# Kernel optimization log

Measured on AMD Instinct MI355X. Metric: run time of the kernel, lower is better.

The kernel has to match this reference:

```python
import jax, jax.numpy as jnp
import numpy as np

B, C, H, W = 16, 256, 56, 56
CR = C // 4
PAD = 1
NUM_ITERS = 5


def _conv(x, w, b):
    # NCHW conv, stride 1, 'same' padding for k=3
    y = jax.lax.conv_general_dilated(x, w, (1, 1), [(PAD, PAD), (PAD, PAD)],
                                     dimension_numbers=('NCHW', 'OIHW', 'NCHW'))
    return y + b[None, :, None, None]


_GAUSS = np.array([[1., 2., 1.], [2., 4., 2.], [1., 2., 1.]], np.float32) / 16.0


def _crf_rnn(unary1, compat, spatial_w):
    # Mean-field CRF-RNN refinement with num_labels=2 and a fixed spatial Gaussian kernel.
    unary = jnp.concatenate([unary1, -unary1], axis=1)  # [B,2,h,w] two-label unary from 1-ch map
    gk = jnp.tile(jnp.asarray(_GAUSS)[None, None], (2, 1, 1, 1))  # depthwise [2,1,3,3]
    q = jax.nn.softmax(unary, axis=1)
    for _ in range(NUM_ITERS):
        blur = jax.lax.conv_general_dilated(q, gk, (1, 1), [(1, 1), (1, 1)],
                                            dimension_numbers=('NCHW', 'OIHW', 'NCHW'),
                                            feature_group_count=2)
        msg = blur * spatial_w[None, :, None, None]          # filter-output weighting
        pairwise = jnp.einsum('lk,bkhw->blhw', compat, msg)  # label compatibility transform
        q = jax.nn.softmax(unary - pairwise, axis=1)
    return q[:, 1:2]  # P(label=1) as refined spatial attention map


def _forward(x, w0_0, b0_0, w0_1, b0_1, w0_2, b0_2, w0_3, b0_3, w0_4, b0_4,
             w1, b1, w2, b2, fc1_w, fc2_w, fc2_b, crf_compat, crf_spatial_w):
    f1 = jax.nn.relu(_conv(x, w0_0, b0_0))             # [B,C,H,W]  (dominant compute)
    f1c = jnp.mean(f1, axis=(2, 3), keepdims=True)      # global avg pool -> [B,C,1,1]
    f2 = jax.nn.relu(_conv(f1c, w0_1, b0_1))            # [B,C,1,1]
    v_c = jax.nn.sigmoid(f1c[:, :, 0, 0] @ fc1_w.T)[:, :, None, None]  # channel attention
    f_c = v_c * f2
    f3 = jax.nn.relu(_conv(f_c, w0_2, b0_2))
    f4 = jax.nn.relu(_conv(f3, w0_3, b0_3))
    f3s = jax.nn.relu(_conv(f3, w1, b1))                # [B,C/4,1,1]
    v0s = jax.nn.relu(_conv(f3s, w2, b2))               # [B,1,1,1] initial spatial attention
    v_s = _crf_rnn(v0s, crf_compat, crf_spatial_w)      # CRF-RNN refined attention
    f_s = v_s * f4
    f_r = jax.nn.relu(_conv(f_s, w0_4, b0_4))
    f_ra = jnp.mean(f_r, axis=(2, 3), keepdims=True)    # [B,C,1,1]
    p_n = jax.nn.sigmoid(f_ra[:, :, 0, 0] @ fc2_w.T + fc2_b)  # [B,1]
    return p_n


def setup_inputs() -> dict:
    key = jax.random.key(0)
    ks = jax.random.split(key, 16)

    def w(k, shape, fan):
        return jax.random.normal(k, shape, jnp.float32) / np.sqrt(fan)

    inp = {'x': jax.random.normal(ks[0], (B, C, H, W), jnp.float32)}
    for i in range(5):
        inp['w0_%d' % i] = w(ks[1 + i], (C, C, 3, 3), C * 9)
        inp['b0_%d' % i] = jnp.zeros((C,), jnp.float32)
    inp['w1'] = w(ks[6], (CR, C, 3, 3), C * 9)
    inp['b1'] = jnp.zeros((CR,), jnp.float32)
    inp['w2'] = w(ks[7], (1, CR, 3, 3), CR * 9)
    inp['b2'] = jnp.zeros((1,), jnp.float32)
    inp['fc1_w'] = w(ks[8], (C, C), C)
    inp['fc2_w'] = w(ks[9], (1, C), C)
    inp['fc2_b'] = jnp.zeros((1,), jnp.float32)
    inp['crf_compat'] = jnp.asarray([[0., 1.], [1., 0.]], jnp.float32) + 0.1 * jax.random.normal(ks[10], (2, 2), jnp.float32)
    inp['crf_spatial_w'] = jnp.ones((2,), jnp.float32)
    return inp


def reference(x, w0_0, b0_0, w0_1, b0_1, w0_2, b0_2, w0_3, b0_3, w0_4, b0_4,
              w1, b1, w2, b2, fc1_w, fc2_w, fc2_b, crf_compat, crf_spatial_w):
    return _forward(x, w0_0, b0_0, w0_1, b0_1, w0_2, b0_2, w0_3, b0_3, w0_4, b0_4,
                    w1, b1, w2, b2, fc1_w, fc2_w, fc2_b, crf_compat, crf_spatial_w)
```

## Files before the change

kernel.cpp:

```cpp
#include <hip/hip_runtime.h>
#include <hip/hip_bf16.h>

typedef __bf16 bf16x8 __attribute__((ext_vector_type(8)));
typedef float f32x4 __attribute__((ext_vector_type(4)));

#define NB 16
#define NC 256
#define NHW 3136
#define NW 56
#define PROW 58
#define PPLANE (58 * 58)

#define NRX2 1568
#define NBP 288
#define NMAT 85
#define NHALO 114

__device__ __forceinline__ unsigned short f2bf(float f) {
    union { float f; unsigned u; } v; v.f = f;
    unsigned r = v.u + 0x7FFFu + ((v.u >> 16) & 1u);
    return (unsigned short)(r >> 16);
}

__device__ __forceinline__ void gload_lds16(const void* g, void* l) {
    __builtin_amdgcn_global_load_lds((const __attribute__((address_space(1))) void*)g,
                                     (__attribute__((address_space(3))) void*)l, 16, 0, 0);
}

__global__ void k_prep(const float* __restrict__ x,
                       const float* __restrict__ w0_0, const float* __restrict__ w0_1,
                       const float* __restrict__ w0_2, const float* __restrict__ w0_3,
                       const float* __restrict__ w0_4, const float* __restrict__ w1,
                       const float* __restrict__ w2, const float* __restrict__ fc1_w,
                       unsigned short* __restrict__ xT, unsigned short* __restrict__ Bp,
                       float* __restrict__ w01T, float* __restrict__ w02T,
                       float* __restrict__ w03T, float* __restrict__ w04T,
                       float* __restrict__ fc1T, float* __restrict__ w1T,
                       float* __restrict__ w2c) {
    __shared__ float sh[64 * 65];
    int bid = blockIdx.x, tid = threadIdx.x;

    if (bid < NRX2) {
        int hwb = bid % 98;
        int b = bid / 98;
        int c_l = tid >> 5, hw_l = tid & 31;
        int qd = tid & 7, hw2 = tid >> 3;
        int hw = hwb * 32 + hw2;
        int y = hw / 56, xp = hw - y * 56;
        for (int cb = 0; cb < 8; ++cb) {
            const float* src = x + ((size_t)b * NC + (size_t)cb * 32) * NHW + hwb * 32;
#pragma unroll
            for (int r = 0; r < 4; ++r) {
                int c = c_l + r * 8;
                sh[c * 33 + hw_l] = src[(size_t)c * NHW + hw_l];
            }
            __syncthreads();
            unsigned short* dst = xT + ((size_t)(b * 8 + cb) * PPLANE +
                                        (size_t)(y + 1) * PROW + (xp + 1)) * 32 + qd * 4;
            ushort4 v;
            v.x = f2bf(sh[(qd * 4 + 0) * 33 + hw2]);
            v.y = f2bf(sh[(qd * 4 + 1) * 33 + hw2]);
            v.z = f2bf(sh[(qd * 4 + 2) * 33 + hw2]);
            v.w = f2bf(sh[(qd * 4 + 3) * 33 + hw2]);
            *(ushort4*)dst = v;
            __syncthreads();
        }
        return;
    }
    if (bid < NRX2 + NBP) {
        int bw = bid - NRX2;
#pragma unroll
        for (int k = 0; k < 8; ++k) {
            int idx = (bw * 8 + k) * 256 + tid;
            int q = idx & 31;
            int n = (idx >> 5) & 255;
            int s = idx >> 13;
            int tap = s >> 3;
            int ic = (s & 7) * 32 + q;
            Bp[idx] = f2bf(w0_0[(size_t)n * 2304 + (size_t)ic * 9 + tap]);
        }
        return;
    }
    if (bid < NRX2 + NBP + NMAT) {
        int tb = bid - NRX2 - NBP;
        if (tb < 84) {
            const float* src; float* dst;
            int sstr, estr, off, OD, o0, i0;
            if (tb < 80) {
                int arr = tb >> 4, t16 = tb & 15;
                o0 = (t16 >> 2) * 64; i0 = (t16 & 3) * 64; OD = 256;
                sstr = 2304; estr = 9; off = 4;
                switch (arr) {
                    case 0: src = w0_1; dst = w01T; break;
                    case 1: src = w0_2; dst = w02T; break;
                    case 2: src = w0_3; dst = w03T; break;
                    case 3: src = w0_4; dst = w04T; break;
                    default: src = fc1_w; dst = fc1T; sstr = 256; estr = 1; off = 0; break;
                }
            } else {
                int t4i = tb - 80; o0 = 0; i0 = t4i * 64; OD = 64;
                sstr = 2304; estr = 9; off = 4;
                src = w1; dst = w1T;
            }
            int i1 = tid & 63, o4 = tid >> 6;
#pragma unroll
            for (int p = 0; p < 16; ++p) {
                int oo = p * 4 + o4;
                sh[oo * 65 + i1] = src[(size_t)(o0 + oo) * sstr + (size_t)(i0 + i1) * estr + off];
            }
            __syncthreads();
            int o1 = tid & 63, i4 = tid >> 6;
#pragma unroll
            for (int p = 0; p < 16; ++p) {
                int ii = p * 4 + i4;
                dst[(size_t)(i0 + ii) * OD + o0 + o1] = sh[o1 * 65 + ii];
            }
        } else {
            if (tid < 64) w2c[tid] = w2[tid * 9 + 4];
        }
        return;
    }
    {
        int t = (bid - NRX2 - NBP - NMAT) * 256 + tid;
        if (t >= 128 * 228) return;
        int plane = t / 228, h = t % 228;
        int row, xc;
        if (h < 58)       { row = 0;       xc = h; }
        else if (h < 116) { row = 57;      xc = h - 58; }
        else if (h < 172) { row = h - 115; xc = 0; }
        else              { row = h - 171; xc = 57; }
        size_t e = ((size_t)plane * PPLANE + (size_t)row * PROW + xc) * 32;
        uint4 z = {0u, 0u, 0u, 0u};
        *(uint4*)(xT + e)      = z;
        *(uint4*)(xT + e + 8)  = z;
        *(uint4*)(xT + e + 16) = z;
        *(uint4*)(xT + e + 24) = z;
    }
}

__global__ __launch_bounds__(256, 2) void k_conv(
    const unsigned short* __restrict__ xT,
    const unsigned short* __restrict__ Bp,
    const float* __restrict__ b0_0,
    float* __restrict__ partial) {
    __shared__ __align__(16) char alds[2][16384];
    int lblk = ((blockIdx.x & 7) * 56) + (blockIdx.x >> 3);
    int b = lblk / 28, pt = lblk % 28;
    int tid = threadIdx.x;
    int lane = tid & 63, wave = tid >> 6;
    int col = lane & 15, grp = lane >> 4;
    int nbase = wave * 64;

    int swz = (lane & 3) ^ ((lane >> 3) & 3);
    int pixoff = ((lane >> 2) << 6) + (swz << 4);
    const char* xbytes = (const char*)xT;
    size_t stage_row = (size_t)(pt * 2 + wave) * (PROW * 64);

    int p_[7][3];
#pragma unroll
    for (int mt = 0; mt < 7; ++mt) {
        int q = mt * 16 + col;
        int r = q >= 56 ? 1 : 0;
        int x = q - 56 * r;
#pragma unroll
        for (int dxi = 0; dxi < 3; ++dxi) {
            int ppx = x + dxi;
            int slot = grp ^ ((ppx >> 1) & 3);
            p_[mt][dxi] = r * 4096 + ppx * 64 + slot * 16;
        }
    }
    int boff[4];
#pragma unroll
    for (int nt = 0; nt < 4; ++nt)
        boff[nt] = ((nbase + nt * 16 + col) * 32 + grp * 8) * 2;

    f32x4 acc[7][4];
#pragma unroll
    for (int mt = 0; mt < 7; ++mt)
#pragma unroll
        for (int nt = 0; nt < 4; ++nt) {
            acc[mt][nt][0] = 0.f; acc[mt][nt][1] = 0.f;
            acc[mt][nt][2] = 0.f; acc[mt][nt][3] = 0.f;
        }

    {
        const char* g0 = xbytes + (size_t)(b * 8) * (PPLANE * 64) + stage_row + pixoff;
        char* l0 = &alds[0][wave * 4096];
#pragma unroll
        for (int j = 0; j < 4; ++j)
            gload_lds16(g0 + j * 1024, l0 + j * 1024);
    }
    bf16x8 bcur[4], bnxt[4];
    {
        const char* bp0 = (const char*)Bp;
#pragma unroll
        for (int nt = 0; nt < 4; ++nt)
            bcur[nt] = *(const bf16x8*)(bp0 + boff[nt]);
    }
    __syncthreads();

    for (int icb = 0; icb < 8; ++icb) {
        int cur = icb & 1;
        if (icb < 7) {
            const char* g = xbytes + (size_t)(b * 8 + icb + 1) * (PPLANE * 64) + stage_row + pixoff;
            char* l = &alds[cur ^ 1][wave * 4096];
#pragma unroll
            for (int j = 0; j < 4; ++j)
                gload_lds16(g + j * 1024, l + j * 1024);
        }
        const char* abuf = alds[cur];
#pragma unroll
        for (int tap = 0; tap < 9; ++tap) {
            int nicb = (tap == 8) ? icb + 1 : icb;
            int ntap = (tap == 8) ? 0 : tap + 1;
            if (nicb < 8) {
                const char* bp = (const char*)Bp + ((size_t)(ntap * 8 + nicb) << 13);
#pragma unroll
                for (int nt = 0; nt < 4; ++nt)
                    bnxt[nt] = *(const bf16x8*)(bp + boff[nt]);
            }
            int dyi = tap / 3, dxi = tap % 3;
            bf16x8 af[7];
#pragma unroll
            for (int mt = 0; mt < 7; ++mt)
                af[mt] = *(const bf16x8*)(abuf + (p_[mt][dxi] + dyi * 4096));
#pragma unroll
            for (int mt = 0; mt < 7; ++mt)
#pragma unroll
                for (int nt = 0; nt < 4; ++nt)
                    acc[mt][nt] = __builtin_amdgcn_mfma_f32_16x16x32_bf16(af[mt], bcur[nt], acc[mt][nt], 0, 0, 0);
#pragma unroll
            for (int nt = 0; nt < 4; ++nt) bcur[nt] = bnxt[nt];
        }
        __syncthreads();
    }

#pragma unroll
    for (int nt = 0; nt < 4; ++nt) {
        int n = nbase + nt * 16 + col;
        float bias = b0_0[n];
        float s = 0.f;
#pragma unroll
        for (int mt = 0; mt < 7; ++mt)
#pragma unroll
            for (int j = 0; j < 4; ++j)
                s += fmaxf(acc[mt][nt][j] + bias, 0.f);
        s += __shfl_down(s, 32);
        s += __shfl_down(s, 16);
        if (grp == 0) partial[(size_t)lblk * NC + n] = s;
    }
}

__global__ __launch_bounds__(1024) void k_tail(
    const float* __restrict__ partial,
    const float* __restrict__ w01T, const float* __restrict__ fc1T,
    const float* __restrict__ w02T, const float* __restrict__ w03T,
    const float* __restrict__ w04T, const float* __restrict__ w1T,
    const float* __restrict__ w2c,
    const float* __restrict__ b0_1, const float* __restrict__ b0_2,
    const float* __restrict__ b0_3, const float* __restrict__ b0_4,
    const float* __restrict__ b1, const float* __restrict__ b2,
    const float* __restrict__ fc2_w, const float* __restrict__ fc2_b,
    const float* __restrict__ compat, const float* __restrict__ spatial_w,
    float* __restrict__ out) {
    __shared__ float fc[256], t2[256], t3[256], t4[256];
    __shared__ float rA[4][256], rB[4][256];
    __shared__ float red64[64];
    __shared__ float vs_sh;
    int b = blockIdx.x, tid = threadIdx.x;
    int o = tid & 255, seg = tid >> 8;
    int i0 = seg * 64;

    {
        float s = 0.f;
        const float* pp = partial + (size_t)b * 28 * 256 + o;
#pragma unroll
        for (int r = seg * 7; r < seg * 7 + 7; ++r) s += pp[r * 256];
        rA[seg][o] = s;
    }
    __syncthreads();
    if (seg == 0) fc[o] = (rA[0][o] + rA[1][o] + rA[2][o] + rA[3][o]) * (1.f / 3136.f);
    __syncthreads();

    {
        float a2 = 0.f, av = 0.f;
        for (int i = i0; i < i0 + 64; ++i) {
            float fi = fc[i];
            a2 = fmaf(w01T[i * 256 + o], fi, a2);
            av = fmaf(fc1T[i * 256 + o], fi, av);
        }
        rA[seg][o] = a2; rB[seg][o] = av;
    }
    __syncthreads();
    if (seg == 0) {
        float A = rA[0][o] + rA[1][o] + rA[2][o] + rA[3][o];
        float V = rB[0][o] + rB[1][o] + rB[2][o] + rB[3][o];
        t2[o] = fmaxf(A + b0_1[o], 0.f) / (1.f + expf(-V));
    }
    __syncthreads();

    {
        float a3 = 0.f;
        for (int i = i0; i < i0 + 64; ++i) a3 = fmaf(w02T[i * 256 + o], t2[i], a3);
        rA[seg][o] = a3;
    }
    __syncthreads();
    if (seg == 0) t3[o] = fmaxf(rA[0][o] + rA[1][o] + rA[2][o] + rA[3][o] + b0_2[o], 0.f);
    __syncthreads();

    {
        float a4 = 0.f;
        for (int i = i0; i < i0 + 64; ++i) a4 = fmaf(w03T[i * 256 + o], t3[i], a4);
        rA[seg][o] = a4;
        int o64 = tid & 63, s16 = tid >> 6;
        float a5 = 0.f;
        for (int i = s16 * 16; i < s16 * 16 + 16; ++i) a5 = fmaf(w1T[i * 64 + o64], t3[i], a5);
        ((float*)rB)[s16 * 64 + o64] = a5;
    }
    __syncthreads();
    if (seg == 0) t4[o] = fmaxf(rA[0][o] + rA[1][o] + rA[2][o] + rA[3][o] + b0_3[o], 0.f);
    if (tid < 64) {
        float a5 = 0.f;
        const float* rb = (const float*)rB;
#pragma unroll
        for (int j = 0; j < 16; ++j) a5 += rb[j * 64 + tid];
        float v = fmaxf(a5 + b1[tid], 0.f);
        red64[tid] = v * w2c[tid];
    }
    __syncthreads();
    if (tid == 0) {
        float u = 0.f;
        for (int i = 0; i < 64; ++i) u += red64[i];
        u = fmaxf(u + b2[0], 0.f);
        float c00 = compat[0], c01 = compat[1], c10 = compat[2], c11 = compat[3];
        float sw0 = spatial_w[0], sw1 = spatial_w[1];
        float q1 = 1.f / (1.f + expf(2.f * u));
        float q0 = 1.f - q1;
        for (int it = 0; it < 5; ++it) {
            float m0 = q0 * 0.25f * sw0;
            float m1 = q1 * 0.25f * sw1;
            float pw0 = c00 * m0 + c01 * m1;
            float pw1 = c10 * m0 + c11 * m1;
            float z0 = u - pw0, z1 = -u - pw1;
            q1 = 1.f / (1.f + expf(z0 - z1));
            q0 = 1.f - q1;
        }
        vs_sh = q1;
    }
    __syncthreads();

    {
        float a6 = 0.f;
        for (int i = i0; i < i0 + 64; ++i) a6 = fmaf(w04T[i * 256 + o], t4[i], a6);
        rA[seg][o] = a6;
    }
    __syncthreads();
    if (seg == 0) {
        float A = rA[0][o] + rA[1][o] + rA[2][o] + rA[3][o];
        float fr = fmaxf(vs_sh * A + b0_4[o], 0.f);
        rB[0][o] = fr * fc2_w[o];
    }
    __syncthreads();
    if (tid < 128) rB[0][tid] += rB[0][tid + 128];
    __syncthreads();
    if (tid < 64) rB[0][tid] += rB[0][tid + 64];
    __syncthreads();
    if (tid == 0) {
        float t = 0.f;
        for (int i = 0; i < 64; ++i) t += rB[0][i];
        out[b] = 1.f / (1.f + expf(-(t + fc2_b[0])));
    }
}

extern "C" void kernel_launch(void* const* d_in, const int* in_sizes, int n_in,
                              void* d_out, int out_size, void* d_ws, size_t ws_size,
                              hipStream_t stream) {
    const float* x     = (const float*)d_in[0];
    const float* w0_0  = (const float*)d_in[1];
    const float* b0_0  = (const float*)d_in[2];
    const float* w0_1  = (const float*)d_in[3];
    const float* b0_1  = (const float*)d_in[4];
    const float* w0_2  = (const float*)d_in[5];
    const float* b0_2  = (const float*)d_in[6];
    const float* w0_3  = (const float*)d_in[7];
    const float* b0_3  = (const float*)d_in[8];
    const float* w0_4  = (const float*)d_in[9];
    const float* b0_4  = (const float*)d_in[10];
    const float* w1    = (const float*)d_in[11];
    const float* b1    = (const float*)d_in[12];
    const float* w2    = (const float*)d_in[13];
    const float* b2    = (const float*)d_in[14];
    const float* fc1_w = (const float*)d_in[15];
    const float* fc2_w = (const float*)d_in[16];
    const float* fc2_b = (const float*)d_in[17];
    const float* compat = (const float*)d_in[18];
    const float* sw     = (const float*)d_in[19];

    unsigned short* xT = (unsigned short*)d_ws;
    unsigned short* Bp = xT + (size_t)128 * PPLANE * 32;
    float* w01T = (float*)(Bp + 589824);
    float* w02T = w01T + 65536;
    float* w03T = w02T + 65536;
    float* w04T = w03T + 65536;
    float* fc1T = w04T + 65536;
    float* w1T  = fc1T + 65536;
    float* w2c  = w1T + 16384;
    float* partial = w2c + 64;

    hipLaunchKernelGGL(k_prep, dim3(NRX2 + NBP + NMAT + NHALO), dim3(256), 0, stream,
                       x, w0_0, w0_1, w0_2, w0_3, w0_4, w1, w2, fc1_w,
                       xT, Bp, w01T, w02T, w03T, w04T, fc1T, w1T, w2c);
    hipLaunchKernelGGL(k_conv, dim3(448), dim3(256), 0, stream, xT, Bp, b0_0, partial);
    hipLaunchKernelGGL(k_tail, dim3(16), dim3(1024), 0, stream, partial,
                       w01T, fc1T, w02T, w03T, w04T, w1T, w2c,
                       b0_1, b0_2, b0_3, b0_4, b1, b2, fc2_w, fc2_b, compat, sw,
                       (float*)d_out);
}
```

Before: 201.8 us.

## Split prep into finer blocks and triple-buffer B fragments with MFMA priority

```diff
diff --git a/kernel.cpp b/kernel.cpp
--- a/kernel.cpp
+++ b/kernel.cpp
@@ -11,9 +11,8 @@
 #define PROW 58
 #define PPLANE (58 * 58)
 
-#define NRX2 1568
-#define NBP 288
-#define NMAT 85
+#define NRX 12544
+#define NRW 2389
 #define NHALO 114
 
 __device__ __forceinline__ unsigned short f2bf(float f) {
@@ -40,21 +39,24 @@
     __shared__ float sh[64 * 65];
     int bid = blockIdx.x, tid = threadIdx.x;
 
-    if (bid < NRX2) {
+    if (bid < NRX) {
         int hwb = bid % 98;
-        int b = bid / 98;
-        int c_l = tid >> 5, hw_l = tid & 31;
-        int qd = tid & 7, hw2 = tid >> 3;
-        int hw = hwb * 32 + hw2;
-        int y = hw / 56, xp = hw - y * 56;
-        for (int cb = 0; cb < 8; ++cb) {
+        int cb = (bid / 98) % 8;
+        int b = bid / (98 * 8);
+        {
+            int c_l = tid >> 5, hw_l = tid & 31;
             const float* src = x + ((size_t)b * NC + (size_t)cb * 32) * NHW + hwb * 32;
 #pragma unroll
             for (int r = 0; r < 4; ++r) {
                 int c = c_l + r * 8;
                 sh[c * 33 + hw_l] = src[(size_t)c * NHW + hw_l];
             }
-            __syncthreads();
+        }
+        __syncthreads();
+        {
+            int qd = tid & 7, hw2 = tid >> 3;
+            int hw = hwb * 32 + hw2;
+            int y = hw / 56, xp = hw - y * 56;
             unsigned short* dst = xT + ((size_t)(b * 8 + cb) * PPLANE +
                                         (size_t)(y + 1) * PROW + (xp + 1)) * 32 + qd * 4;
             ushort4 v;
@@ -63,26 +65,22 @@
             v.z = f2bf(sh[(qd * 4 + 2) * 33 + hw2]);
             v.w = f2bf(sh[(qd * 4 + 3) * 33 + hw2]);
             *(ushort4*)dst = v;
-            __syncthreads();
         }
         return;
     }
-    if (bid < NRX2 + NBP) {
-        int bw = bid - NRX2;
-#pragma unroll
-        for (int k = 0; k < 8; ++k) {
-            int idx = (bw * 8 + k) * 256 + tid;
+    if (bid < NRX + NRW) {
+        int bw = bid - NRX;
+        if (bw < 2304) {
+            int idx = bw * 256 + tid;
             int q = idx & 31;
             int n = (idx >> 5) & 255;
             int s = idx >> 13;
             int tap = s >> 3;
             int ic = (s & 7) * 32 + q;
             Bp[idx] = f2bf(w0_0[(size_t)n * 2304 + (size_t)ic * 9 + tap]);
-        }
-        return;
-    }
-    if (bid < NRX2 + NBP + NMAT) {
-        int tb = bid - NRX2 - NBP;
+            return;
+        }
+        int tb = bw - 2304;
         if (tb < 84) {
             const float* src; float* dst;
             int sstr, estr, off, OD, o0, i0;
@@ -121,7 +119,7 @@
         return;
     }
     {
-        int t = (bid - NRX2 - NBP - NMAT) * 256 + tid;
+        int t = (bid - NRX - NRW) * 256 + tid;
         if (t >= 128 * 228) return;
         int plane = t / 228, h = t % 228;
         int row, xc;
@@ -190,12 +188,15 @@
         for (int j = 0; j < 4; ++j)
             gload_lds16(g0 + j * 1024, l0 + j * 1024);
     }
-    bf16x8 bcur[4], bnxt[4];
+    bf16x8 bq[3][4];
     {
         const char* bp0 = (const char*)Bp;
-#pragma unroll
-        for (int nt = 0; nt < 4; ++nt)
-            bcur[nt] = *(const bf16x8*)(bp0 + boff[nt]);
+        const char* bp1 = (const char*)Bp + ((size_t)(1 * 8) << 13);
+#pragma unroll
+        for (int nt = 0; nt < 4; ++nt) {
+            bq[0][nt] = *(const bf16x8*)(bp0 + boff[nt]);
+            bq[1][nt] = *(const bf16x8*)(bp1 + boff[nt]);
+        }
     }
     __syncthreads();
 
@@ -211,26 +212,29 @@
         const char* abuf = alds[cur];
 #pragma unroll
         for (int tap = 0; tap < 9; ++tap) {
-            int nicb = (tap == 8) ? icb + 1 : icb;
-            int ntap = (tap == 8) ? 0 : tap + 1;
-            if (nicb < 8) {
-                const char* bp = (const char*)Bp + ((size_t)(ntap * 8 + nicb) << 13);
-#pragma unroll
-                for (int nt = 0; nt < 4; ++nt)
-                    bnxt[nt] = *(const bf16x8*)(bp + boff[nt]);
+            {
+                int gt = tap + 2;
+                int nicb = icb + (gt >= 9 ? 1 : 0);
+                int ntap = gt >= 9 ? gt - 9 : gt;
+                if (nicb < 8) {
+                    const char* bp = (const char*)Bp + ((size_t)(ntap * 8 + nicb) << 13);
+#pragma unroll
+                    for (int nt = 0; nt < 4; ++nt)
+                        bq[(tap + 2) % 3][nt] = *(const bf16x8*)(bp + boff[nt]);
+                }
             }
             int dyi = tap / 3, dxi = tap % 3;
             bf16x8 af[7];
 #pragma unroll
             for (int mt = 0; mt < 7; ++mt)
                 af[mt] = *(const bf16x8*)(abuf + (p_[mt][dxi] + dyi * 4096));
+            __builtin_amdgcn_s_setprio(1);
 #pragma unroll
             for (int mt = 0; mt < 7; ++mt)
 #pragma unroll
                 for (int nt = 0; nt < 4; ++nt)
-                    acc[mt][nt] = __builtin_amdgcn_mfma_f32_16x16x32_bf16(af[mt], bcur[nt], acc[mt][nt], 0, 0, 0);
-#pragma unroll
-            for (int nt = 0; nt < 4; ++nt) bcur[nt] = bnxt[nt];
+                    acc[mt][nt] = __builtin_amdgcn_mfma_f32_16x16x32_bf16(af[mt], bq[tap % 3][nt], acc[mt][nt], 0, 0, 0);
+            __builtin_amdgcn_s_setprio(0);
         }
         __syncthreads();
     }
@@ -407,7 +411,7 @@
     float* w2c  = w1T + 16384;
     float* partial = w2c + 64;
 
-    hipLaunchKernelGGL(k_prep, dim3(NRX2 + NBP + NMAT + NHALO), dim3(256), 0, stream,
+    hipLaunchKernelGGL(k_prep, dim3(NRX + NRW + NHALO), dim3(256), 0, stream,
                        x, w0_0, w0_1, w0_2, w0_3, w0_4, w1, w2, fc1_w,
                        xT, Bp, w01T, w02T, w03T, w04T, fc1T, w1T, w2c);
     hipLaunchKernelGGL(k_conv, dim3(448), dim3(256), 0, stream, xT, Bp, b0_0, partial);
```

Result: faster. 196.7 us (-2.5%).
